# Optimization experiments

Measured on AMD Instinct MI355X. Metric: run time of the kernel, lower is better.

Reference implementation:

```python
import jax, jax.numpy as jnp
import numpy as np
from jax import lax

# Fixed high-pass biquad coefficients from SpecTransform.__init__ (a0=b0=1)
A_HP = (-1.99599, 0.996)
B_HP = (-2.0, 1.0)


def _biquad(x, b0, b1, b2, a1, a2):
    """Direct-form-I second-order IIR along last axis of x: (B, T).
    y[t] = b0*x[t] + b1*x[t-1] + b2*x[t-2] - a1*y[t-1] - a2*y[t-2]
    Matches torchaudio.functional.biquad (which calls lfilter with
    default clamp=True, clipping the final output to [-1, 1]).
    """
    z = jnp.zeros((x.shape[0],), x.dtype)

    def step(carry, xt):
        x1, x2, y1, y2 = carry
        y = b0 * xt + b1 * x1 + b2 * x2 - a1 * y1 - a2 * y2
        return (xt, x1, y, y1), y

    _, y = lax.scan(step, (z, z, z, z), x.T)  # scan over time, carry over batch
    return jnp.clip(y.T, -1.0, 1.0)


def _chain(sig, coefs):
    # coefs = [a1, a2, b1, b2] from _rand_resp (hoisted out for determinism)
    a1, a2, b1, b2 = coefs[0], coefs[1], coefs[2], coefs[3]
    sig = _biquad(sig, 1.0, B_HP[0], B_HP[1], A_HP[0], A_HP[1])
    sig = _biquad(sig, 1.0, b1, b2, a1, a2)
    return sig


def setup_inputs() -> dict:
    key = jax.random.key(0)
    k1, k2, k3, k4 = jax.random.split(key, 4)
    B, T = 64, 160000  # 64 clips of 10 s @ 16 kHz
    x = jax.random.normal(k1, (B, T), jnp.float32) * 0.1
    n = jax.random.normal(k2, (B, T), jnp.float32) * 0.1
    # 0.75 * (U[0,1) - 0.5), same distribution as _rand_resp
    coef_x = (jax.random.uniform(k3, (4,), jnp.float32) - 0.5) * 0.75
    coef_n = (jax.random.uniform(k4, (4,), jnp.float32) - 0.5) * 0.75
    return {"x": x, "n": n, "coef_x": coef_x, "coef_n": coef_n}


def reference(x, n, coef_x, coef_n):
    return (_chain(x, coef_x), _chain(n, coef_n))
```

## Files before the change

kernel.cpp:

```cpp
#include <hip/hip_runtime.h>
#include <math.h>

#define T_LEN   160000
#define NROW    128
#define CH      32
#define NCH     5000
#define OWNT    20
#define O_CH    256
#define TILES   20
#define NBLK    (NROW * TILES)
#define SLOTS   258
#define NF4     (SLOTS * 8)

#define C1_HP ( 1.99599)
#define C2_HP (-0.996)
#define C1F   ( 1.99599f)
#define C2F   (-0.996f)

__device__ __forceinline__ int swz4(int F) { return F ^ ((F >> 3) & 7); }
__device__ __forceinline__ float clip1f(float v) { return fminf(fmaxf(v, -1.0f), 1.0f); }

__global__ __launch_bounds__(256) void pass_a1(const float* __restrict__ x,
                                               const float* __restrict__ nn,
                                               double2* __restrict__ e1) {
  int g = blockIdx.x * blockDim.x + threadIdx.x;
  if (g >= NROW * NCH) return;
  int row = g / NCH, c = g % NCH;
  const float* src = (row < 64) ? (x + (size_t)row * T_LEN)
                                : (nn + (size_t)(row - 64) * T_LEN);
  const float* xp = src + c * CH;
  float x1 = 0.f, x2 = 0.f;
  if (c) { x1 = xp[-1]; x2 = xp[-2]; }
  double y1 = 0.0, y2 = 0.0;
#pragma unroll
  for (int j = 0; j < CH; j += 4) {
    float4 xv = *reinterpret_cast<const float4*>(xp + j);
#define A1STEP(XF) { float xt = (XF); \
    float fir = (xt - 2.f * x1 + x2); \
    double y = (double)fir + (C1_HP * y1 + C2_HP * y2); \
    x2 = x1; x1 = xt; y2 = y1; y1 = y; }
    A1STEP(xv.x) A1STEP(xv.y) A1STEP(xv.z) A1STEP(xv.w)
#undef A1STEP
  }
  e1[g] = make_double2(y1, y2);
}

__global__ __launch_bounds__(256) void scan_row(const double2* __restrict__ e,
                                                float2* __restrict__ s) {
  __shared__ double wm[4][6];
  const int t = threadIdx.x, row = blockIdx.x;
  const int lane = t & 63, wv = t >> 6;
  double pm2 = 0.0, pm1 = 0.0, p0 = 1.0;
#pragma unroll
  for (int k = 1; k <= CH; ++k) {
    double pn = C1_HP * p0 + C2_HP * pm1;
    pm2 = pm1; pm1 = p0; p0 = pn;
  }
  const double m00 = p0,  m01 = C2_HP * pm1;
  const double m10 = pm1, m11 = C2_HP * pm2;
  const double2* ep = e + (size_t)row * NCH;
  const int base = t * OWNT;
  double f1 = 0.0, f2 = 0.0;
  for (int j = 0; j < OWNT; ++j) {
    int c = base + j;
    double2 ev = (c < NCH) ? ep[c] : make_double2(0.0, 0.0);
    double n1 = m00 * f1 + m01 * f2 + ev.x;
    double n2 = m10 * f1 + m11 * f2 + ev.y;
    f1 = n1; f2 = n2;
  }
  double b00 = m00, b01 = m01, b10 = m10, b11 = m11;
  double r00 = 1.0, r01 = 0.0, r10 = 0.0, r11 = 1.0;
  int ee = OWNT;
  while (ee) {
    if (ee & 1) {
      double t00 = b00 * r00 + b01 * r10, t01 = b00 * r01 + b01 * r11;
      double t10 = b10 * r00 + b11 * r10, t11 = b10 * r01 + b11 * r11;
      r00 = t00; r01 = t01; r10 = t10; r11 = t11;
    }
    double q00 = b00 * b00 + b01 * b10, q01 = b00 * b01 + b01 * b11;
    double q10 = b10 * b00 + b11 * b10, q11 = b10 * b01 + b11 * b11;
    b00 = q00; b01 = q01; b10 = q10; b11 = q11;
    ee >>= 1;
  }
  double P00 = r00, P01 = r01, P10 = r10, P11 = r11, V1 = f1, V2 = f2;
#pragma unroll
  for (int off = 1; off < 64; off <<= 1) {
    double u00 = __shfl_up(P00, off), u01 = __shfl_up(P01, off);
    double u10 = __shfl_up(P10, off), u11 = __shfl_up(P11, off);
    double uv1 = __shfl_up(V1, off),  uv2 = __shfl_up(V2, off);
    if (lane >= off) {
      double nv1 = P00 * uv1 + P01 * uv2 + V1;
      double nv2 = P10 * uv1 + P11 * uv2 + V2;
      double n00 = P00 * u00 + P01 * u10, n01 = P00 * u01 + P01 * u11;
      double n10 = P10 * u00 + P11 * u10, n11 = P10 * u01 + P11 * u11;
      P00 = n00; P01 = n01; P10 = n10; P11 = n11; V1 = nv1; V2 = nv2;
    }
  }
  if (lane == 63) {
    wm[wv][0] = P00; wm[wv][1] = P01; wm[wv][2] = P10; wm[wv][3] = P11;
    wm[wv][4] = V1;  wm[wv][5] = V2;
  }
  __syncthreads();
  double S1 = 0.0, S2 = 0.0;
  for (int w = 0; w < wv; ++w) {
    double n1 = wm[w][0] * S1 + wm[w][1] * S2 + wm[w][4];
    double n2 = wm[w][2] * S1 + wm[w][3] * S2 + wm[w][5];
    S1 = n1; S2 = n2;
  }
  double q00 = __shfl_up(P00, 1), q01 = __shfl_up(P01, 1);
  double q10 = __shfl_up(P10, 1), q11 = __shfl_up(P11, 1);
  double qv1 = __shfl_up(V1, 1),  qv2 = __shfl_up(V2, 1);
  double st1, st2;
  if (lane == 0) { st1 = S1; st2 = S2; }
  else { st1 = q00 * S1 + q01 * S2 + qv1; st2 = q10 * S1 + q11 * S2 + qv2; }
  float2* sp = s + (size_t)row * NCH;
  double s1v = st1, s2v = st2;
  for (int j = 0; j < OWNT; ++j) {
    int c = base + j;
    if (c < NCH) {
      sp[c] = make_float2((float)s1v, (float)s2v);
      double2 ev = ep[c];
      double n1 = m00 * s1v + m01 * s2v + ev.x;
      double n2 = m10 * s1v + m11 * s2v + ev.y;
      s1v = n1; s2v = n2;
    }
  }
}

__global__ __launch_bounds__(256) void emit_kernel(const float* __restrict__ x,
                                                   const float* __restrict__ nn,
                                                   const float2* __restrict__ s1,
                                                   const float* __restrict__ cx,
                                                   const float* __restrict__ cn,
                                                   float* __restrict__ out) {
  __shared__ float4 xs4[NF4];
  const int tid = threadIdx.x;
  const int b = blockIdx.x;
  const int row = b / TILES, tile = b % TILES;
  const int c0 = tile * O_CH;
  const long g0 = (long)(c0 - 2) * CH;
  const float* src = (row < 64) ? x + (size_t)row * T_LEN
                                : nn + (size_t)(row - 64) * T_LEN;
  const float2* srow = s1 + (size_t)row * NCH;

  for (int k = tid; k < NF4; k += 256) {
    long gi = g0 + 4L * k;
    float4 v = make_float4(0.f, 0.f, 0.f, 0.f);
    if (gi >= 0 && gi < T_LEN) v = *reinterpret_cast<const float4*>(src + gi);
    xs4[swz4(k)] = v;
  }
  __syncthreads();

  const float* cf = (row < 64) ? cx : cn;
  const float A1c = cf[0], A2c = cf[1], B1c = cf[2], B2c = cf[3];
  const int c = c0 + tid;
  const bool act = (c < NCH);

  float4 o[8];

#define WSTEP(XT) { float xt_ = (XT); \
    float fir = (xt_ - 2.f * x1 + x2) + (C1F * y1 + C2F * y2); \
    x2 = x1; x1 = xt_; y2 = y1; y1 = fir; \
    float vv = clip1f(fir); \
    float zz = vv + B1c * v1 + B2c * v2 - A1c * z1 - A2c * z2; \
    v2 = v1; v1 = vv; z2 = z1; z1 = zz; }
#define ESTEP(XT, OT) { float xt_ = (XT); \
    float fir = (xt_ - 2.f * x1 + x2) + (C1F * y1 + C2F * y2); \
    x2 = x1; x1 = xt_; y2 = y1; y1 = fir; \
    float vv = clip1f(fir); \
    float zz = vv + B1c * v1 + B2c * v2 - A1c * z1 - A2c * z2; \
    v2 = v1; v1 = vv; z2 = z1; z1 = zz; OT = clip1f(zz); }

  if (act) {
    float y1 = 0.f, y2 = 0.f, x1 = 0.f, x2 = 0.f;
    float v1 = 0.f, v2 = 0.f, z1 = 0.f, z2 = 0.f;
    const int cw = (c >= 2) ? (c - 2) : 0;
    if (cw > 0) {
      float2 sv = srow[cw];
      y1 = sv.x; y2 = sv.y;
      v1 = clip1f(sv.x); v2 = clip1f(sv.y);
      const long gb = (long)cw * CH;
      x1 = src[gb - 1]; x2 = src[gb - 2];
    }
#pragma unroll
    for (int si = 0; si < 2; ++si) {
      const int cc = c - 2 + si;
      if (cc >= 0) {
        const int slot = tid + si;
        float4 a[8];
#pragma unroll
        for (int q = 0; q < 8; ++q) a[q] = xs4[swz4(slot * 8 + q)];
#pragma unroll
        for (int q = 0; q < 8; ++q) {
          WSTEP(a[q].x) WSTEP(a[q].y) WSTEP(a[q].z) WSTEP(a[q].w)
        }
      }
    }
    {
      const int slot = tid + 2;
#pragma unroll
      for (int q = 0; q < 8; ++q) o[q] = xs4[swz4(slot * 8 + q)];
#pragma unroll
      for (int q = 0; q < 8; ++q) {
        ESTEP(o[q].x, o[q].x) ESTEP(o[q].y, o[q].y)
        ESTEP(o[q].z, o[q].z) ESTEP(o[q].w, o[q].w)
      }
    }
  }
#undef WSTEP
#undef ESTEP
  __syncthreads();
  if (act) {
    const int slot = tid + 2;
#pragma unroll
    for (int q = 0; q < 8; ++q) xs4[swz4(slot * 8 + q)] = o[q];
  }
  __syncthreads();

  float* orow = out + (size_t)row * T_LEN;
  const long tile_start = (long)c0 * CH;
  for (int k = tid; k < O_CH * 8; k += 256) {
    long gi = tile_start + 4L * k;
    if (gi < T_LEN)
      *reinterpret_cast<float4*>(orow + gi) = xs4[swz4(16 + k)];
  }
}

extern "C" void kernel_launch(void* const* d_in, const int* in_sizes, int n_in,
                              void* d_out, int out_size, void* d_ws, size_t ws_size,
                              hipStream_t stream) {
  const float* x  = (const float*)d_in[0];
  const float* nn = (const float*)d_in[1];
  const float* cx = (const float*)d_in[2];
  const float* cn = (const float*)d_in[3];
  float* out = (float*)d_out;

  double2* e1 = (double2*)d_out;
  float2*  s1 = (float2*)d_ws;

  const int total = NROW * NCH;
  const int blk = 256;
  const int nb = (total + blk - 1) / blk;

  pass_a1<<<nb, blk, 0, stream>>>(x, nn, e1);
  scan_row<<<NROW, blk, 0, stream>>>(e1, s1);
  emit_kernel<<<NBLK, blk, 0, stream>>>(x, nn, s1, cx, cn, out);
}
```

Measured before the change: 74.50 us.

## Replace redundant warmup recompute with cross-thread state exchange in emit kernel

Previously each thread in the emit kernel re-ran both biquads over two preceding chunks as warmup, which tripled the sequential work. Now each thread runs the first filter once over its own chunk. It takes the neighbour's clipped tail via shuffles and shared memory, then runs the second filter from zero state. A final pass adds the homogeneous response propagated from the previous two chunks' end states. Tile size drops to 252 chunks plus 2 halo threads within 256 threads, and launch bounds request 5 blocks per CU. The cost is two extra barriers and float-precision approximation of the second filter's state propagation across two chunks.

```diff
diff --git a/kernel.cpp b/kernel.cpp
--- a/kernel.cpp
+++ b/kernel.cpp
@@ -6,11 +6,11 @@
 #define CH      32
 #define NCH     5000
 #define OWNT    20
-#define O_CH    256
+#define O_CH    252
+#define SLOTS   254
+#define NF4     (SLOTS * 8)
 #define TILES   20
 #define NBLK    (NROW * TILES)
-#define SLOTS   258
-#define NF4     (SLOTS * 8)
 
 #define C1_HP ( 1.99599)
 #define C2_HP (-0.996)
@@ -127,13 +127,15 @@
   }
 }
 
-__global__ __launch_bounds__(256) void emit_kernel(const float* __restrict__ x,
-                                                   const float* __restrict__ nn,
-                                                   const float2* __restrict__ s1,
-                                                   const float* __restrict__ cx,
-                                                   const float* __restrict__ cn,
-                                                   float* __restrict__ out) {
+__global__ __launch_bounds__(256, 5) void emit_kernel(const float* __restrict__ x,
+                                                      const float* __restrict__ nn,
+                                                      const float2* __restrict__ s1,
+                                                      const float* __restrict__ cx,
+                                                      const float* __restrict__ cn,
+                                                      float* __restrict__ out) {
   __shared__ float4 xs4[NF4];
+  __shared__ float2 smt[4];
+  __shared__ float2 sme[8];
   const int tid = threadIdx.x;
   const int b = blockIdx.x;
   const int row = b / TILES, tile = b % TILES;
@@ -142,6 +144,8 @@
   const float* src = (row < 64) ? x + (size_t)row * T_LEN
                                 : nn + (size_t)(row - 64) * T_LEN;
   const float2* srow = s1 + (size_t)row * NCH;
+  const float* cf = (row < 64) ? cx : cn;
+  const float A1c = cf[0], A2c = cf[1], B1c = cf[2], B2c = cf[3];
 
   for (int k = tid; k < NF4; k += 256) {
     long gi = g0 + 4L * k;
@@ -151,69 +155,112 @@
   }
   __syncthreads();
 
-  const float* cf = (row < 64) ? cx : cn;
-  const float A1c = cf[0], A2c = cf[1], B1c = cf[2], B2c = cf[3];
-  const int c = c0 + tid;
-  const bool act = (c < NCH);
-
-  float4 o[8];
-
-#define WSTEP(XT) { float xt_ = (XT); \
-    float fir = (xt_ - 2.f * x1 + x2) + (C1F * y1 + C2F * y2); \
-    x2 = x1; x1 = xt_; y2 = y1; y1 = fir; \
-    float vv = clip1f(fir); \
-    float zz = vv + B1c * v1 + B2c * v2 - A1c * z1 - A2c * z2; \
-    v2 = v1; v1 = vv; z2 = z1; z1 = zz; }
-#define ESTEP(XT, OT) { float xt_ = (XT); \
-    float fir = (xt_ - 2.f * x1 + x2) + (C1F * y1 + C2F * y2); \
-    x2 = x1; x1 = xt_; y2 = y1; y1 = fir; \
-    float vv = clip1f(fir); \
-    float zz = vv + B1c * v1 + B2c * v2 - A1c * z1 - A2c * z2; \
-    v2 = v1; v1 = vv; z2 = z1; z1 = zz; OT = clip1f(zz); }
+  const int lane = tid & 63, wv = tid >> 6;
+  int slot, chunk;
+  if (tid < O_CH) { slot = tid + 2; chunk = c0 + tid; }
+  else if (tid < O_CH + 2) { slot = tid - O_CH; chunk = c0 - 2 + slot; }
+  else { slot = -1; chunk = NCH; }
+  const bool act = (slot >= 0) && (chunk >= 0) && (chunk < NCH);
+
+  float4 v4[8];
+  float tail_x = 0.f, tail_y = 0.f;
+  float ez1 = 0.f, ez2 = 0.f;
 
   if (act) {
     float y1 = 0.f, y2 = 0.f, x1 = 0.f, x2 = 0.f;
-    float v1 = 0.f, v2 = 0.f, z1 = 0.f, z2 = 0.f;
-    const int cw = (c >= 2) ? (c - 2) : 0;
-    if (cw > 0) {
-      float2 sv = srow[cw];
+    if (chunk > 0) {
+      float2 sv = srow[chunk];
       y1 = sv.x; y2 = sv.y;
+      if (slot >= 1) {
+        float4 pt = xs4[swz4((slot - 1) * 8 + 7)];
+        x1 = pt.w; x2 = pt.z;
+      } else {
+        long gb = (long)chunk * CH;
+        x1 = src[gb - 1]; x2 = src[gb - 2];
+      }
+    }
+#pragma unroll
+    for (int q = 0; q < 8; ++q) {
+      float4 a = xs4[swz4(slot * 8 + q)];
+      float4 o;
+#define A1S(XT, OT) { float xt_ = (XT); \
+      float yy = (xt_ - 2.f * x1 + x2) + (C1F * y1 + C2F * y2); \
+      x2 = x1; x1 = xt_; y2 = y1; y1 = yy; OT = clip1f(yy); }
+      A1S(a.x, o.x) A1S(a.y, o.y) A1S(a.z, o.z) A1S(a.w, o.w)
+#undef A1S
+      v4[q] = o;
+    }
+    tail_x = v4[7].w; tail_y = v4[7].z;
+    if (lane == 63 && wv < 3) smt[wv + 1] = make_float2(tail_x, tail_y);
+    if (tid == O_CH + 1)      smt[0]      = make_float2(tail_x, tail_y);
+  }
+  __syncthreads();
+
+  if (act) {
+    float v1, v2;
+    if (slot == 0) {
+      float2 sv = srow[chunk];
       v1 = clip1f(sv.x); v2 = clip1f(sv.y);
-      const long gb = (long)cw * CH;
-      x1 = src[gb - 1]; x2 = src[gb - 2];
-    }
-#pragma unroll
-    for (int si = 0; si < 2; ++si) {
-      const int cc = c - 2 + si;
-      if (cc >= 0) {
-        const int slot = tid + si;
-        float4 a[8];
-#pragma unroll
-        for (int q = 0; q < 8; ++q) a[q] = xs4[swz4(slot * 8 + q)];
-#pragma unroll
-        for (int q = 0; q < 8; ++q) {
-          WSTEP(a[q].x) WSTEP(a[q].y) WSTEP(a[q].z) WSTEP(a[q].w)
-        }
-      }
-    }
-    {
-      const int slot = tid + 2;
-#pragma unroll
-      for (int q = 0; q < 8; ++q) o[q] = xs4[swz4(slot * 8 + q)];
-#pragma unroll
-      for (int q = 0; q < 8; ++q) {
-        ESTEP(o[q].x, o[q].x) ESTEP(o[q].y, o[q].y)
-        ESTEP(o[q].z, o[q].z) ESTEP(o[q].w, o[q].w)
-      }
-    }
-  }
-#undef WSTEP
-#undef ESTEP
-  __syncthreads();
-  if (act) {
-    const int slot = tid + 2;
-#pragma unroll
-    for (int q = 0; q < 8; ++q) xs4[swz4(slot * 8 + q)] = o[q];
+    } else {
+      float ux = __shfl_up(tail_x, 1);
+      float uy = __shfl_up(tail_y, 1);
+      if (lane == 0) { float2 tb = smt[wv]; ux = tb.x; uy = tb.y; }
+      v1 = ux; v2 = uy;
+    }
+    if (chunk == 0) { v1 = 0.f; v2 = 0.f; }
+    float z1 = 0.f, z2 = 0.f;
+#pragma unroll
+    for (int q = 0; q < 8; ++q) {
+      float4 t = v4[q];
+      float4 o;
+#define BS(VV, OT) { float vv_ = (VV); \
+      float zz = vv_ + B1c * v1 + B2c * v2 - A1c * z1 - A2c * z2; \
+      v2 = v1; v1 = vv_; z2 = z1; z1 = zz; OT = zz; }
+      BS(t.x, o.x) BS(t.y, o.y) BS(t.z, o.z) BS(t.w, o.w)
+#undef BS
+      v4[q] = o;
+    }
+    ez1 = z1; ez2 = z2;
+    if (lane >= 62 && wv < 3) sme[2 * (wv + 1) + (lane & 1)] = make_float2(ez1, ez2);
+    if (tid >= O_CH && tid < O_CH + 2) sme[tid - O_CH] = make_float2(ez1, ez2);
+  }
+  __syncthreads();
+
+  if (tid < O_CH && act) {
+    float pm2 = 0.f, pm1 = 0.f, p0 = 1.f;
+#pragma unroll
+    for (int k = 0; k < CH; ++k) {
+      float pn = -A1c * p0 - A2c * pm1;
+      pm2 = pm1; pm1 = p0; p0 = pn;
+    }
+    const float m00 = p0,  m01 = -A2c * pm1;
+    const float m10 = pm1, m11 = -A2c * pm2;
+    float u1x = __shfl_up(ez1, 1), u1y = __shfl_up(ez2, 1);
+    float u2x = __shfl_up(ez1, 2), u2y = __shfl_up(ez2, 2);
+    if (lane == 0) {
+      float2 a = sme[2 * wv + 1]; u1x = a.x; u1y = a.y;
+      float2 bq = sme[2 * wv];    u2x = bq.x; u2y = bq.y;
+    } else if (lane == 1) {
+      float2 bq = sme[2 * wv + 1]; u2x = bq.x; u2y = bq.y;
+    }
+    float s2x, s2y;
+    if (chunk == 0)      { s2x = 0.f; s2y = 0.f; }
+    else if (chunk == 1) { s2x = u1x; s2y = u1y; }
+    else {
+      s2x = u1x + m00 * u2x + m01 * u2y;
+      s2y = u1y + m10 * u2x + m11 * u2y;
+    }
+    float h1 = s2x, h2 = s2y;
+#pragma unroll
+    for (int q = 0; q < 8; ++q) {
+      float4 t = v4[q];
+      float4 o;
+#define CS(ZB, OT) { float hh = -A1c * h1 - A2c * h2; \
+      OT = clip1f((ZB) + hh); h2 = h1; h1 = hh; }
+      CS(t.x, o.x) CS(t.y, o.y) CS(t.z, o.z) CS(t.w, o.w)
+#undef CS
+      xs4[swz4(slot * 8 + q)] = o;
+    }
   }
   __syncthreads();
 
```

Result: faster. 65.93 us (-11.5%).

## Replace LDS-tiled emit with per-chunk direct loads and linear state correction

Applied to the files above, without the earlier changes.

The emit kernel no longer stages input tiles in shared memory with swizzling and barriers. Each thread reads its own chunk straight from global memory. Instead of warming the second filter up from zero state over two preceding chunks, it computes zero-state end states for the two preceding chunks and joins them with a 32-step transition matrix to get an approximate start state for its chunk. The partial-state buffer also shrinks from double2 to float2, which halves that traffic. The cost is uncoalesced strided global loads and stores (each thread touches 128 contiguous bytes) and extra numerical approximation, because the second filter ignores the clip nonlinearity and history older than two chunks.

```diff
diff --git a/kernel.cpp b/kernel.cpp
--- a/kernel.cpp
+++ b/kernel.cpp
@@ -6,23 +6,17 @@
 #define CH      32
 #define NCH     5000
 #define OWNT    20
-#define O_CH    256
-#define TILES   20
-#define NBLK    (NROW * TILES)
-#define SLOTS   258
-#define NF4     (SLOTS * 8)
 
 #define C1_HP ( 1.99599)
 #define C2_HP (-0.996)
 #define C1F   ( 1.99599f)
 #define C2F   (-0.996f)
 
-__device__ __forceinline__ int swz4(int F) { return F ^ ((F >> 3) & 7); }
 __device__ __forceinline__ float clip1f(float v) { return fminf(fmaxf(v, -1.0f), 1.0f); }
 
 __global__ __launch_bounds__(256) void pass_a1(const float* __restrict__ x,
                                                const float* __restrict__ nn,
-                                               double2* __restrict__ e1) {
+                                               float2* __restrict__ e1) {
   int g = blockIdx.x * blockDim.x + threadIdx.x;
   if (g >= NROW * NCH) return;
   int row = g / NCH, c = g % NCH;
@@ -42,10 +36,10 @@
     A1STEP(xv.x) A1STEP(xv.y) A1STEP(xv.z) A1STEP(xv.w)
 #undef A1STEP
   }
-  e1[g] = make_double2(y1, y2);
-}
-
-__global__ __launch_bounds__(256) void scan_row(const double2* __restrict__ e,
+  e1[g] = make_float2((float)y1, (float)y2);
+}
+
+__global__ __launch_bounds__(256) void scan_row(const float2* __restrict__ e,
                                                 float2* __restrict__ s) {
   __shared__ double wm[4][6];
   const int t = threadIdx.x, row = blockIdx.x;
@@ -58,14 +52,14 @@
   }
   const double m00 = p0,  m01 = C2_HP * pm1;
   const double m10 = pm1, m11 = C2_HP * pm2;
-  const double2* ep = e + (size_t)row * NCH;
+  const float2* ep = e + (size_t)row * NCH;
   const int base = t * OWNT;
   double f1 = 0.0, f2 = 0.0;
   for (int j = 0; j < OWNT; ++j) {
     int c = base + j;
-    double2 ev = (c < NCH) ? ep[c] : make_double2(0.0, 0.0);
-    double n1 = m00 * f1 + m01 * f2 + ev.x;
-    double n2 = m10 * f1 + m11 * f2 + ev.y;
+    float2 ev = (c < NCH) ? ep[c] : make_float2(0.f, 0.f);
+    double n1 = m00 * f1 + m01 * f2 + (double)ev.x;
+    double n2 = m10 * f1 + m11 * f2 + (double)ev.y;
     f1 = n1; f2 = n2;
   }
   double b00 = m00, b01 = m01, b10 = m10, b11 = m11;
@@ -119,9 +113,9 @@
     int c = base + j;
     if (c < NCH) {
       sp[c] = make_float2((float)s1v, (float)s2v);
-      double2 ev = ep[c];
-      double n1 = m00 * s1v + m01 * s2v + ev.x;
-      double n2 = m10 * s1v + m11 * s2v + ev.y;
+      float2 ev = ep[c];
+      double n1 = m00 * s1v + m01 * s2v + (double)ev.x;
+      double n2 = m10 * s1v + m11 * s2v + (double)ev.y;
       s1v = n1; s2v = n2;
     }
   }
@@ -133,97 +127,102 @@
                                                    const float* __restrict__ cx,
                                                    const float* __restrict__ cn,
                                                    float* __restrict__ out) {
-  __shared__ float4 xs4[NF4];
-  const int tid = threadIdx.x;
-  const int b = blockIdx.x;
-  const int row = b / TILES, tile = b % TILES;
-  const int c0 = tile * O_CH;
-  const long g0 = (long)(c0 - 2) * CH;
-  const float* src = (row < 64) ? x + (size_t)row * T_LEN
-                                : nn + (size_t)(row - 64) * T_LEN;
+  int g = blockIdx.x * blockDim.x + threadIdx.x;
+  if (g >= NROW * NCH) return;
+  int row = g / NCH, c = g % NCH;
+  const float* src = (row < 64) ? (x + (size_t)row * T_LEN)
+                                : (nn + (size_t)(row - 64) * T_LEN);
   const float2* srow = s1 + (size_t)row * NCH;
-
-  for (int k = tid; k < NF4; k += 256) {
-    long gi = g0 + 4L * k;
-    float4 v = make_float4(0.f, 0.f, 0.f, 0.f);
-    if (gi >= 0 && gi < T_LEN) v = *reinterpret_cast<const float4*>(src + gi);
-    xs4[swz4(k)] = v;
-  }
-  __syncthreads();
-
   const float* cf = (row < 64) ? cx : cn;
   const float A1c = cf[0], A2c = cf[1], B1c = cf[2], B2c = cf[3];
-  const int c = c0 + tid;
-  const bool act = (c < NCH);
-
-  float4 o[8];
-
-#define WSTEP(XT) { float xt_ = (XT); \
-    float fir = (xt_ - 2.f * x1 + x2) + (C1F * y1 + C2F * y2); \
-    x2 = x1; x1 = xt_; y2 = y1; y1 = fir; \
-    float vv = clip1f(fir); \
+
+  float pm2 = 0.f, pm1 = 0.f, p0 = 1.f;
+#pragma unroll
+  for (int k = 0; k < CH; ++k) {
+    float pn = -A1c * p0 - A2c * pm1;
+    pm2 = pm1; pm1 = p0; p0 = pn;
+  }
+  const float m00 = p0,  m01 = -A2c * pm1;
+  const float m10 = pm1, m11 = -A2c * pm2;
+
+#define AB(XT) { float xt_ = (XT); \
+    float yy = (xt_ - 2.f * x1 + x2) + (C1F * y1 + C2F * y2); \
+    x2 = x1; x1 = xt_; y2 = y1; y1 = yy; \
+    float vv = clip1f(yy); \
     float zz = vv + B1c * v1 + B2c * v2 - A1c * z1 - A2c * z2; \
     v2 = v1; v1 = vv; z2 = z1; z1 = zz; }
-#define ESTEP(XT, OT) { float xt_ = (XT); \
-    float fir = (xt_ - 2.f * x1 + x2) + (C1F * y1 + C2F * y2); \
-    x2 = x1; x1 = xt_; y2 = y1; y1 = fir; \
-    float vv = clip1f(fir); \
-    float zz = vv + B1c * v1 + B2c * v2 - A1c * z1 - A2c * z2; \
-    v2 = v1; v1 = vv; z2 = z1; z1 = zz; OT = clip1f(zz); }
-
-  if (act) {
-    float y1 = 0.f, y2 = 0.f, x1 = 0.f, x2 = 0.f;
-    float v1 = 0.f, v2 = 0.f, z1 = 0.f, z2 = 0.f;
-    const int cw = (c >= 2) ? (c - 2) : 0;
-    if (cw > 0) {
-      float2 sv = srow[cw];
-      y1 = sv.x; y2 = sv.y;
-      v1 = clip1f(sv.x); v2 = clip1f(sv.y);
-      const long gb = (long)cw * CH;
-      x1 = src[gb - 1]; x2 = src[gb - 2];
-    }
-#pragma unroll
-    for (int si = 0; si < 2; ++si) {
-      const int cc = c - 2 + si;
-      if (cc >= 0) {
-        const int slot = tid + si;
-        float4 a[8];
-#pragma unroll
-        for (int q = 0; q < 8; ++q) a[q] = xs4[swz4(slot * 8 + q)];
-#pragma unroll
-        for (int q = 0; q < 8; ++q) {
-          WSTEP(a[q].x) WSTEP(a[q].y) WSTEP(a[q].z) WSTEP(a[q].w)
-        }
-      }
-    }
-    {
-      const int slot = tid + 2;
-#pragma unroll
-      for (int q = 0; q < 8; ++q) o[q] = xs4[swz4(slot * 8 + q)];
-#pragma unroll
-      for (int q = 0; q < 8; ++q) {
-        ESTEP(o[q].x, o[q].x) ESTEP(o[q].y, o[q].y)
-        ESTEP(o[q].z, o[q].z) ESTEP(o[q].w, o[q].w)
-      }
-    }
-  }
-#undef WSTEP
-#undef ESTEP
-  __syncthreads();
-  if (act) {
-    const int slot = tid + 2;
-#pragma unroll
-    for (int q = 0; q < 8; ++q) xs4[swz4(slot * 8 + q)] = o[q];
-  }
-  __syncthreads();
-
-  float* orow = out + (size_t)row * T_LEN;
-  const long tile_start = (long)c0 * CH;
-  for (int k = tid; k < O_CH * 8; k += 256) {
-    long gi = tile_start + 4L * k;
-    if (gi < T_LEN)
-      *reinterpret_cast<float4*>(orow + gi) = xs4[swz4(16 + k)];
-  }
+
+  float e2ax = 0.f, e2ay = 0.f, e2bx = 0.f, e2by = 0.f;
+  float tlx = 0.f, tly = 0.f;
+
+  if (c >= 2) {
+    const int k = c - 2;
+    const long gb = (long)k * CH;
+    float4 a[8];
+#pragma unroll
+    for (int q = 0; q < 8; ++q) a[q] = *reinterpret_cast<const float4*>(src + gb + 4 * q);
+    float y1 = 0.f, y2 = 0.f, x1 = 0.f, x2 = 0.f, v1 = 0.f, v2 = 0.f;
+    if (k > 0) {
+      float2 sv = srow[k];
+      y1 = sv.x; y2 = sv.y; v1 = clip1f(sv.x); v2 = clip1f(sv.y);
+      float2 tp = *reinterpret_cast<const float2*>(src + gb - 2);
+      x2 = tp.x; x1 = tp.y;
+    }
+    float z1 = 0.f, z2 = 0.f;
+#pragma unroll
+    for (int q = 0; q < 8; ++q) { AB(a[q].x) AB(a[q].y) AB(a[q].z) AB(a[q].w) }
+    e2ax = z1; e2ay = z2;
+    tlx = a[7].w; tly = a[7].z;
+  }
+  if (c >= 1) {
+    const int k = c - 1;
+    const long gb = (long)k * CH;
+    float4 a[8];
+#pragma unroll
+    for (int q = 0; q < 8; ++q) a[q] = *reinterpret_cast<const float4*>(src + gb + 4 * q);
+    float y1 = 0.f, y2 = 0.f, x1 = 0.f, x2 = 0.f, v1 = 0.f, v2 = 0.f;
+    if (k > 0) {
+      float2 sv = srow[k];
+      y1 = sv.x; y2 = sv.y; v1 = clip1f(sv.x); v2 = clip1f(sv.y);
+      x1 = tlx; x2 = tly;
+    }
+    float z1 = 0.f, z2 = 0.f;
+#pragma unroll
+    for (int q = 0; q < 8; ++q) { AB(a[q].x) AB(a[q].y) AB(a[q].z) AB(a[q].w) }
+    e2bx = z1; e2by = z2;
+    tlx = a[7].w; tly = a[7].z;
+  }
+  float s2x, s2y;
+  if (c == 0)      { s2x = 0.f; s2y = 0.f; }
+  else if (c == 1) { s2x = e2bx; s2y = e2by; }
+  else {
+    s2x = e2bx + m00 * e2ax + m01 * e2ay;
+    s2y = e2by + m10 * e2ax + m11 * e2ay;
+  }
+  {
+    const long gb = (long)c * CH;
+    float4 a[8];
+#pragma unroll
+    for (int q = 0; q < 8; ++q) a[q] = *reinterpret_cast<const float4*>(src + gb + 4 * q);
+    float y1 = 0.f, y2 = 0.f, x1 = 0.f, x2 = 0.f, v1 = 0.f, v2 = 0.f;
+    if (c > 0) {
+      float2 sv = srow[c];
+      y1 = sv.x; y2 = sv.y; v1 = clip1f(sv.x); v2 = clip1f(sv.y);
+      x1 = tlx; x2 = tly;
+    }
+    float z1 = s2x, z2 = s2y;
+    float* op = out + (size_t)row * T_LEN + gb;
+#pragma unroll
+    for (int q = 0; q < 8; ++q) {
+      float4 o;
+      AB(a[q].x) o.x = clip1f(z1);
+      AB(a[q].y) o.y = clip1f(z1);
+      AB(a[q].z) o.z = clip1f(z1);
+      AB(a[q].w) o.w = clip1f(z1);
+      *reinterpret_cast<float4*>(op + 4 * q) = o;
+    }
+  }
+#undef AB
 }
 
 extern "C" void kernel_launch(void* const* d_in, const int* in_sizes, int n_in,
@@ -235,8 +234,8 @@
   const float* cn = (const float*)d_in[3];
   float* out = (float*)d_out;
 
-  double2* e1 = (double2*)d_out;
-  float2*  s1 = (float2*)d_ws;
+  float2* e1 = (float2*)d_out;
+  float2* s1 = (float2*)d_ws;
 
   const int total = NROW * NCH;
   const int blk = 256;
@@ -244,5 +243,5 @@
 
   pass_a1<<<nb, blk, 0, stream>>>(x, nn, e1);
   scan_row<<<NROW, blk, 0, stream>>>(e1, s1);
-  emit_kernel<<<NBLK, blk, 0, stream>>>(x, nn, s1, cx, cn, out);
-}
+  emit_kernel<<<nb, blk, 0, stream>>>(x, nn, s1, cx, cn, out);
+}
```

Result: slower. 92.64 us (+24.3%).
